# Optimization experiments

Measured on AMD Instinct MI355X. Metric: run time of the kernel, lower is better.

Reference implementation:

```python
import jax, jax.numpy as jnp
import numpy as np

N_NODES = 50000
N_EDGES = 640000
D = 128      # in_feats
OUT = 128    # out_feats


def setup_inputs() -> dict:
    key = jax.random.key(0)
    ks = jax.random.split(key, 8)
    feat = jax.random.normal(ks[0], (N_NODES, D), dtype=jnp.float32)
    weight = jax.random.uniform(ks[1], (N_EDGES,), dtype=jnp.float32)
    src = jax.random.randint(ks[2], (N_EDGES,), 0, N_NODES, dtype=jnp.int64)
    dst = jax.random.randint(ks[3], (N_EDGES,), 0, N_NODES, dtype=jnp.int64)
    # xavier_uniform with relu gain ~ sqrt(2)*sqrt(6/(fan_in+fan_out))
    g = np.sqrt(2.0)
    lim_pool = g * np.sqrt(6.0 / (D + D))
    lim_neigh = g * np.sqrt(6.0 / (2 * D + OUT))
    W_pool = jax.random.uniform(ks[4], (D, D), dtype=jnp.float32, minval=-lim_pool, maxval=lim_pool)
    b_pool = jnp.zeros((D,), dtype=jnp.float32)
    W_neigh = jax.random.uniform(ks[5], (OUT, 2 * D), dtype=jnp.float32, minval=-lim_neigh, maxval=lim_neigh)
    b_neigh = jnp.zeros((OUT,), dtype=jnp.float32)
    return {"feat": feat, "weight": weight, "src": src, "dst": dst,
            "W_pool": W_pool, "b_pool": b_pool, "W_neigh": W_neigh, "b_neigh": b_neigh}


def reference(feat, weight, src, dst, W_pool, b_pool, W_neigh, b_neigh):
    n = feat.shape[0]
    # fc_pool: h = feat @ W_pool.T + b_pool  -> [N, D]
    h = feat @ W_pool.T + b_pool
    # u_mul_e: per-edge message m_e = h[src_e] * w_e  -> [E, D]
    m = h[src] * weight[:, None]
    # max reduce over incoming edges (scatter-max by dst)
    neigh = jax.ops.segment_max(m, dst, num_segments=n)
    # zero-degree nodes get 0 (segment_max fills empties with -inf)
    deg = jax.ops.segment_sum(jnp.ones_like(weight), dst, num_segments=n)
    neigh = jnp.where(deg[:, None] > 0, neigh, jnp.zeros((), dtype=feat.dtype))
    # fc_neigh on concat(feat, neigh)
    rst = jnp.concatenate([feat, neigh], axis=1) @ W_neigh.T + b_neigh
    return rst
```

## Files before the change

### kernel.cpp

```cpp
#include <hip/hip_runtime.h>
#include <cstdint>
#include <cstddef>

#define N_NODES 50000
#define N_EDGES 640000
#define DF 128

#define NBUCK 196
#define BCAP  6144
#define PA_BLOCKS 250

typedef __attribute__((ext_vector_type(8))) short bf16x8;
typedef __attribute__((ext_vector_type(4))) float f32x4;

__device__ inline unsigned short f2bf(float f) {
    unsigned int u = __float_as_uint(f);
    return (unsigned short)((u + 0x7fffu + ((u >> 16) & 1u)) >> 16);
}

#define NF4 (N_NODES * DF / 4)
#define NWG (3 * 2048)
__global__ __launch_bounds__(256) void k1_setup_bucket(
    const float* __restrict__ feat,
    const float* __restrict__ W_pool,
    const float* __restrict__ W_neigh,
    const int* __restrict__ src,
    const int* __restrict__ dst,
    const float* __restrict__ w,
    unsigned short* __restrict__ featb,
    unsigned short* __restrict__ Wp_f,
    unsigned short* __restrict__ Wn1_f,
    unsigned short* __restrict__ Wn2_f,
    int* __restrict__ bucketcnt,
    uint2* __restrict__ staging)
{
    int bid = blockIdx.x;
    int t = threadIdx.x;
    if (bid < PA_BLOCKS) {
        __shared__ int cnt[NBUCK];
        __shared__ int runbase[NBUCK];
        int base = bid * 2560;
        if (t < NBUCK) cnt[t] = 0;
        __syncthreads();
        uint2 rec[10];
        int bk[10];
        #pragma unroll
        for (int i = 0; i < 10; ++i) {
            int e = base + i * 256 + t;
            int s = src[e], d = dst[e];
            bk[i] = d >> 8;
            rec[i].x = (unsigned int)s | ((unsigned int)(d & 255) << 16);
            rec[i].y = __float_as_uint(w[e]);
            atomicAdd(&cnt[bk[i]], 1);
        }
        __syncthreads();
        if (t < NBUCK) {
            runbase[t] = atomicAdd(&bucketcnt[t], cnt[t]);
            cnt[t] = 0;
        }
        __syncthreads();
        #pragma unroll
        for (int i = 0; i < 10; ++i) {
            int r = atomicAdd(&cnt[bk[i]], 1);
            int pos = runbase[bk[i]] + r;
            if (pos < BCAP) staging[bk[i] * BCAP + pos] = rec[i];
        }
    } else if (bid < 250 + NF4 / 256) {
        int idx = (bid - PA_BLOCKS) * 256 + t;
        float4 v = ((const float4*)feat)[idx];
        ushort4 o;
        o.x = f2bf(v.x); o.y = f2bf(v.y); o.z = f2bf(v.z); o.w = f2bf(v.w);
        ((ushort4*)featb)[idx] = o;
    } else {
        int g = (bid - PA_BLOCKS - NF4 / 256) * 256 + t;
        int m = g >> 11;
        int r8 = g & 2047;
        int L = r8 & 63, tt = (r8 >> 6) & 3, c = r8 >> 8;
        int o = c * 16 + (L & 15);
        int kb = tt * 32 + (L >> 4) * 8;
        const float* srcp;
        unsigned short* dstp;
        if (m == 0)      { srcp = W_pool  + o * 128 + kb;       dstp = Wp_f;  }
        else if (m == 1) { srcp = W_neigh + o * 256 + kb;       dstp = Wn1_f; }
        else             { srcp = W_neigh + o * 256 + 128 + kb; dstp = Wn2_f; }
        ushort4 lo, hi;
        float4 a = ((const float4*)srcp)[0];
        float4 b = ((const float4*)srcp)[1];
        lo.x = f2bf(a.x); lo.y = f2bf(a.y); lo.z = f2bf(a.z); lo.w = f2bf(a.w);
        hi.x = f2bf(b.x); hi.y = f2bf(b.y); hi.z = f2bf(b.z); hi.w = f2bf(b.w);
        ((ushort4*)(dstp + r8 * 8))[0] = lo;
        ((ushort4*)(dstp + r8 * 8))[1] = hi;
    }
}

#define GEMMB 196
__global__ __launch_bounds__(1024) void k2_gemm_passb(
    const unsigned short* __restrict__ featb,
    const unsigned short* __restrict__ Wp_f,
    const float* __restrict__ b_pool,
    unsigned short* __restrict__ hb,
    const int* __restrict__ bucketcnt,
    const uint2* __restrict__ staging,
    int* __restrict__ offsets,
    uint2* __restrict__ edges)
{
    int t = threadIdx.x;
    if (blockIdx.x < GEMMB) {
        int wave = blockIdx.x * 16 + (t >> 6);
        int lane = t & 63;
        int m0 = wave * 16;
        if (m0 >= N_NODES) return;
        const int n = lane & 15, quad = lane >> 4;

        f32x4 acc[8];
        #pragma unroll
        for (int c = 0; c < 8; ++c) {
            float bv = b_pool[c * 16 + n];
            acc[c] = (f32x4){bv, bv, bv, bv};
        }
        const unsigned short* aptr = featb + (size_t)(m0 + n) * DF + quad * 8;
        #pragma unroll
        for (int tt = 0; tt < 4; ++tt) {
            bf16x8 af = *(const bf16x8*)(aptr + tt * 32);
            #pragma unroll
            for (int c = 0; c < 8; ++c) {
                bf16x8 bf = *(const bf16x8*)(Wp_f + (size_t)((c * 4 + tt) * 64 + lane) * 8);
                acc[c] = __builtin_amdgcn_mfma_f32_16x16x32_bf16(af, bf, acc[c], 0, 0, 0);
            }
        }
        #pragma unroll
        for (int c = 0; c < 8; ++c)
            #pragma unroll
            for (int r = 0; r < 4; ++r)
                hb[(size_t)(m0 + quad * 4 + r) * DF + c * 16 + n] = f2bf(acc[c][r]);
    } else {
        __shared__ int dcnt[256];
        __shared__ int sc[256];
        __shared__ int bc[256];
        int b = blockIdx.x - GEMMB;

        if (t < 256) { dcnt[t] = 0; bc[t] = (t < NBUCK) ? bucketcnt[t] : 0; sc[t] = (t < NBUCK) ? bc[t] : 0; }
        __syncthreads();
        #pragma unroll
        for (int off = 1; off < 256; off <<= 1) {
            int u = (t < 256 && t >= off) ? sc[t - off] : 0;
            __syncthreads();
            if (t < 256) sc[t] += u;
            __syncthreads();
        }
        int mybase = (b > 0) ? sc[b - 1] : 0;
        int cnt = bc[b];
        __syncthreads();

        uint2 rec[6];
        int nit = (cnt + 1023) >> 10;
        for (int i = 0; i < nit; ++i) {
            int idx = i * 1024 + t;
            if (idx < cnt) {
                rec[i] = staging[(size_t)b * BCAP + idx];
                atomicAdd(&dcnt[(rec[i].x >> 16) & 255], 1);
            }
        }
        __syncthreads();
        if (t < 256) sc[t] = dcnt[t];
        __syncthreads();
        #pragma unroll
        for (int off = 1; off < 256; off <<= 1) {
            int u = (t < 256 && t >= off) ? sc[t - off] : 0;
            __syncthreads();
            if (t < 256) sc[t] += u;
            __syncthreads();
        }
        if (t < 256) {
            int node = b * 256 + t;
            int excl = sc[t] - dcnt[t];
            if (node < N_NODES) offsets[node] = mybase + excl;
            dcnt[t] = mybase + excl;
        }
        if (b == NBUCK - 1 && t == 0) offsets[N_NODES] = mybase + cnt;
        __syncthreads();
        for (int i = 0; i < nit; ++i) {
            int idx = i * 1024 + t;
            if (idx < cnt) {
                int dl = (rec[i].x >> 16) & 255;
                int pos = atomicAdd(&dcnt[dl], 1);
                uint2 fin;
                fin.x = rec[i].x & 0xFFFFu;
                fin.y = rec[i].y;
                edges[pos] = fin;
            }
        }
    }
}

__global__ __launch_bounds__(1024) void fused_max_out(
    const unsigned short* __restrict__ featb,
    const unsigned short* __restrict__ hb,
    const int* __restrict__ offsets,
    const uint2* __restrict__ edges,
    const unsigned short* __restrict__ Wn1_f,
    const unsigned short* __restrict__ Wn2_f,
    const float* __restrict__ bias,
    float* __restrict__ out)
{
    __shared__ __align__(16) unsigned short nsh[16 * DF];
    const int t = threadIdx.x;
    const int lane = t & 63;
    const int wid = t >> 6;
    const int m0 = blockIdx.x * 16;
    const int half = lane >> 5;
    const int q = lane & 31;

    const int node = __builtin_amdgcn_readfirstlane(m0 + wid);
    int beg = offsets[node], end = offsets[node + 1];
    float4 mx = make_float4(-3.4e38f, -3.4e38f, -3.4e38f, -3.4e38f);

    for (int e = beg; e < end; e += 8) {
        int i1 = min(e + 1, end - 1);
        int i2 = min(e + 2, end - 1);
        int i3 = min(e + 3, end - 1);
        int i4 = min(e + 4, end - 1);
        int i5 = min(e + 5, end - 1);
        int i6 = min(e + 6, end - 1);
        int i7 = min(e + 7, end - 1);
        uint2 e0 = edges[e],  e1 = edges[i1], e2 = edges[i2], e3 = edges[i3];
        uint2 e4 = edges[i4], e5 = edges[i5], e6 = edges[i6], e7 = edges[i7];
        uint2 mA = half ? e1 : e0;
        uint2 mB = half ? e3 : e2;
        uint2 mC = half ? e5 : e4;
        uint2 mD = half ? e7 : e6;
        float wA = __uint_as_float(mA.y);
        float wB = __uint_as_float(mB.y);
        float wC = __uint_as_float(mC.y);
        float wD = __uint_as_float(mD.y);
        uint2 pA = *(const uint2*)(hb + (size_t)mA.x * DF + q * 4);
        uint2 pB = *(const uint2*)(hb + (size_t)mB.x * DF + q * 4);
        uint2 pC = *(const uint2*)(hb + (size_t)mC.x * DF + q * 4);
        uint2 pD = *(const uint2*)(hb + (size_t)mD.x * DF + q * 4);
        mx.x = fmaxf(mx.x, __uint_as_float(pA.x << 16)          * wA);
        mx.y = fmaxf(mx.y, __uint_as_float(pA.x & 0xffff0000u)  * wA);
        mx.z = fmaxf(mx.z, __uint_as_float(pA.y << 16)          * wA);
        mx.w = fmaxf(mx.w, __uint_as_float(pA.y & 0xffff0000u)  * wA);
        mx.x = fmaxf(mx.x, __uint_as_float(pB.x << 16)          * wB);
        mx.y = fmaxf(mx.y, __uint_as_float(pB.x & 0xffff0000u)  * wB);
        mx.z = fmaxf(mx.z, __uint_as_float(pB.y << 16)          * wB);
        mx.w = fmaxf(mx.w, __uint_as_float(pB.y & 0xffff0000u)  * wB);
        mx.x = fmaxf(mx.x, __uint_as_float(pC.x << 16)          * wC);
        mx.y = fmaxf(mx.y, __uint_as_float(pC.x & 0xffff0000u)  * wC);
        mx.z = fmaxf(mx.z, __uint_as_float(pC.y << 16)          * wC);
        mx.w = fmaxf(mx.w, __uint_as_float(pC.y & 0xffff0000u)  * wC);
        mx.x = fmaxf(mx.x, __uint_as_float(pD.x << 16)          * wD);
        mx.y = fmaxf(mx.y, __uint_as_float(pD.x & 0xffff0000u)  * wD);
        mx.z = fmaxf(mx.z, __uint_as_float(pD.y << 16)          * wD);
        mx.w = fmaxf(mx.w, __uint_as_float(pD.y & 0xffff0000u)  * wD);
    }

    float4 o;
    o.x = fmaxf(mx.x, __shfl_xor(mx.x, 32));
    o.y = fmaxf(mx.y, __shfl_xor(mx.y, 32));
    o.z = fmaxf(mx.z, __shfl_xor(mx.z, 32));
    o.w = fmaxf(mx.w, __shfl_xor(mx.w, 32));
    if (beg == end) o = make_float4(0.f, 0.f, 0.f, 0.f);
    if (half == 0) {
        ushort4 ob;
        ob.x = f2bf(o.x); ob.y = f2bf(o.y); ob.z = f2bf(o.z); ob.w = f2bf(o.w);
        int boff = wid * 256 + ((q * 8) ^ ((wid & 7) << 4));
        *(ushort4*)((char*)nsh + boff) = ob;
    }

    const int n = lane & 15, quad = lane >> 4;
    f32x4 acc;
    if (wid < 8) {
        const int c = wid;
        float bv = bias[c * 16 + n];
        acc = (f32x4){bv, bv, bv, bv};
        const unsigned short* a0 = featb + (size_t)(m0 + n) * DF + quad * 8;
        #pragma unroll
        for (int tt = 0; tt < 4; ++tt) {
            bf16x8 af = *(const bf16x8*)(a0 + tt * 32);
            bf16x8 bfv = *(const bf16x8*)(Wn1_f + (size_t)((c * 4 + tt) * 64 + lane) * 8);
            acc = __builtin_amdgcn_mfma_f32_16x16x32_bf16(af, bfv, acc, 0, 0, 0);
        }
    }

    __syncthreads();
    if (wid >= 8) return;

    const int c = wid;
    #pragma unroll
    for (int tt = 0; tt < 4; ++tt) {
        int boff = (quad * 16 + tt * 64) ^ ((n & 7) << 4);
        bf16x8 af = *(const bf16x8*)((const char*)nsh + n * 256 + boff);
        bf16x8 bfv = *(const bf16x8*)(Wn2_f + (size_t)((c * 4 + tt) * 64 + lane) * 8);
        acc = __builtin_amdgcn_mfma_f32_16x16x32_bf16(af, bfv, acc, 0, 0, 0);
    }

    #pragma unroll
    for (int r = 0; r < 4; ++r)
        out[(size_t)(m0 + quad * 4 + r) * DF + c * 16 + n] = acc[r];
}

extern "C" void kernel_launch(void* const* d_in, const int* in_sizes, int n_in,
                              void* d_out, int out_size, void* d_ws, size_t ws_size,
                              hipStream_t stream) {
    const float* feat    = (const float*)d_in[0];
    const float* weight  = (const float*)d_in[1];
    const int*   src     = (const int*)d_in[2];
    const int*   dst     = (const int*)d_in[3];
    const float* W_pool  = (const float*)d_in[4];
    const float* b_pool  = (const float*)d_in[5];
    const float* W_neigh = (const float*)d_in[6];
    const float* b_neigh = (const float*)d_in[7];
    float* out = (float*)d_out;

    char* ws = (char*)d_ws;
    unsigned short* featb  = (unsigned short*)(ws);
    unsigned short* hb     = (unsigned short*)(ws + 12800000);
    unsigned short* Wp_f   = (unsigned short*)(ws + 38400000);
    unsigned short* Wn1_f  = (unsigned short*)(ws + 38432768);
    unsigned short* Wn2_f  = (unsigned short*)(ws + 38465536);
    int*   offsets   = (int*)  (ws + 38498304);
    int*   bucketcnt = (int*)  (ws + 38698368);
    uint2* staging   = (uint2*)(ws + 38699392);
    uint2* edges     = (uint2*)(ws + 48333184);

    hipMemsetAsync(bucketcnt, 0, 1024, stream);

    const int K1_BLOCKS = PA_BLOCKS + NF4 / 256 + NWG / 256;
    k1_setup_bucket<<<K1_BLOCKS, 256, 0, stream>>>(
        feat, W_pool, W_neigh, src, dst, weight,
        featb, Wp_f, Wn1_f, Wn2_f, bucketcnt, staging);

    k2_gemm_passb<<<GEMMB + NBUCK, 1024, 0, stream>>>(
        featb, Wp_f, b_pool, hb, bucketcnt, staging, offsets, edges);

    fused_max_out<<<N_NODES / 16, 1024, 0, stream>>>(
        featb, hb, offsets, edges, Wn1_f, Wn2_f, b_neigh, out);
}
```

Measured before the change: 163.4 us.

## Fuse feature bf16 conversion and pool GEMM into setup kernel

Moves the fc_pool GEMM out of the second kernel and into the first, where each block converts W_pool to bf16 in shared memory and converts feat rows on the fly, writing both featb and hb. This removes the separate featb round trip through global memory before the GEMM and leaves the second kernel doing only the bucket pass. In exchange, every GEMM block redundantly converts the whole 128x128 W_pool into 32KB of LDS, which adds per-block work and may limit occupancy.

After: 176.5 us. 1.08x slower.

```diff
diff --git a/kernel.cpp b/kernel.cpp
--- a/kernel.cpp
+++ b/kernel.cpp
@@ -9,6 +9,8 @@
 #define NBUCK 196
 #define BCAP  6144
 #define PA_BLOCKS 250
+#define GEMM_BLOCKS 782
+#define FRAG_BLOCKS 16
 
 typedef __attribute__((ext_vector_type(8))) short bf16x8;
 typedef __attribute__((ext_vector_type(4))) float f32x4;
@@ -18,17 +20,16 @@
     return (unsigned short)((u + 0x7fffu + ((u >> 16) & 1u)) >> 16);
 }
 
-#define NF4 (N_NODES * DF / 4)
-#define NWG (3 * 2048)
 __global__ __launch_bounds__(256) void k1_setup_bucket(
     const float* __restrict__ feat,
     const float* __restrict__ W_pool,
     const float* __restrict__ W_neigh,
+    const float* __restrict__ b_pool,
     const int* __restrict__ src,
     const int* __restrict__ dst,
     const float* __restrict__ w,
     unsigned short* __restrict__ featb,
-    unsigned short* __restrict__ Wp_f,
+    unsigned short* __restrict__ hb,
     unsigned short* __restrict__ Wn1_f,
     unsigned short* __restrict__ Wn2_f,
     int* __restrict__ bucketcnt,
@@ -65,24 +66,68 @@
             int pos = runbase[bk[i]] + r;
             if (pos < BCAP) staging[bk[i] * BCAP + pos] = rec[i];
         }
-    } else if (bid < 250 + NF4 / 256) {
-        int idx = (bid - PA_BLOCKS) * 256 + t;
-        float4 v = ((const float4*)feat)[idx];
-        ushort4 o;
-        o.x = f2bf(v.x); o.y = f2bf(v.y); o.z = f2bf(v.z); o.w = f2bf(v.w);
-        ((ushort4*)featb)[idx] = o;
+    } else if (bid < PA_BLOCKS + GEMM_BLOCKS) {
+        __shared__ __align__(16) unsigned short wsh[16384];
+        #pragma unroll
+        for (int k = 0; k < 8; ++k) {
+            int r8 = t * 8 + k;
+            int L = r8 & 63, tt2 = (r8 >> 6) & 3, c = r8 >> 8;
+            const float* srcp = W_pool + (c * 16 + (L & 15)) * 128
+                                       + tt2 * 32 + (L >> 4) * 8;
+            float4 a = ((const float4*)srcp)[0];
+            float4 b = ((const float4*)srcp)[1];
+            ushort4 lo, hi;
+            lo.x = f2bf(a.x); lo.y = f2bf(a.y); lo.z = f2bf(a.z); lo.w = f2bf(a.w);
+            hi.x = f2bf(b.x); hi.y = f2bf(b.y); hi.z = f2bf(b.z); hi.w = f2bf(b.w);
+            ((ushort4*)(wsh + r8 * 8))[0] = lo;
+            ((ushort4*)(wsh + r8 * 8))[1] = hi;
+        }
+        __syncthreads();
+
+        int gwave = (bid - PA_BLOCKS) * 4 + (t >> 6);
+        int m0 = gwave * 16;
+        if (m0 < N_NODES) {
+            int lane = t & 63;
+            const int n = lane & 15, quad = lane >> 4;
+            f32x4 acc[8];
+            #pragma unroll
+            for (int c = 0; c < 8; ++c) {
+                float bv = b_pool[c * 16 + n];
+                acc[c] = (f32x4){bv, bv, bv, bv};
+            }
+            const float* fp = feat + (size_t)(m0 + n) * DF + quad * 8;
+            unsigned short* fbp = featb + (size_t)(m0 + n) * DF + quad * 8;
+            #pragma unroll
+            for (int tt = 0; tt < 4; ++tt) {
+                float4 a = ((const float4*)(fp + tt * 32))[0];
+                float4 b = ((const float4*)(fp + tt * 32))[1];
+                union { bf16x8 v; ushort4 u4[2]; } af;
+                af.u4[0].x = f2bf(a.x); af.u4[0].y = f2bf(a.y);
+                af.u4[0].z = f2bf(a.z); af.u4[0].w = f2bf(a.w);
+                af.u4[1].x = f2bf(b.x); af.u4[1].y = f2bf(b.y);
+                af.u4[1].z = f2bf(b.z); af.u4[1].w = f2bf(b.w);
+                *(bf16x8*)(fbp + tt * 32) = af.v;
+                #pragma unroll
+                for (int c = 0; c < 8; ++c) {
+                    bf16x8 bfv = *(const bf16x8*)(wsh + (size_t)((c * 4 + tt) * 64 + lane) * 8);
+                    acc[c] = __builtin_amdgcn_mfma_f32_16x16x32_bf16(af.v, bfv, acc[c], 0, 0, 0);
+                }
+            }
+            #pragma unroll
+            for (int c = 0; c < 8; ++c)
+                #pragma unroll
+                for (int r = 0; r < 4; ++r)
+                    hb[(size_t)(m0 + quad * 4 + r) * DF + c * 16 + n] = f2bf(acc[c][r]);
+        }
     } else {
-        int g = (bid - PA_BLOCKS - NF4 / 256) * 256 + t;
+        int g = (bid - PA_BLOCKS - GEMM_BLOCKS) * 256 + t;
         int m = g >> 11;
         int r8 = g & 2047;
         int L = r8 & 63, tt = (r8 >> 6) & 3, c = r8 >> 8;
         int o = c * 16 + (L & 15);
         int kb = tt * 32 + (L >> 4) * 8;
-        const float* srcp;
-        unsigned short* dstp;
-        if (m == 0)      { srcp = W_pool  + o * 128 + kb;       dstp = Wp_f;  }
-        else if (m == 1) { srcp = W_neigh + o * 256 + kb;       dstp = Wn1_f; }
-        else             { srcp = W_neigh + o * 256 + 128 + kb; dstp = Wn2_f; }
+        const float* srcp = W_neigh + o * 256 + (m ? 128 : 0) + kb;
+        unsigned short* dstp = m ? Wn2_f : Wn1_f;
         ushort4 lo, hi;
         float4 a = ((const float4*)srcp)[0];
         float4 b = ((const float4*)srcp)[1];
@@ -93,102 +138,67 @@
     }
 }
 
-#define GEMMB 196
-__global__ __launch_bounds__(1024) void k2_gemm_passb(
-    const unsigned short* __restrict__ featb,
-    const unsigned short* __restrict__ Wp_f,
-    const float* __restrict__ b_pool,
-    unsigned short* __restrict__ hb,
+__global__ __launch_bounds__(1024) void k2_passb(
     const int* __restrict__ bucketcnt,
     const uint2* __restrict__ staging,
     int* __restrict__ offsets,
     uint2* __restrict__ edges)
 {
     int t = threadIdx.x;
-    if (blockIdx.x < GEMMB) {
-        int wave = blockIdx.x * 16 + (t >> 6);
-        int lane = t & 63;
-        int m0 = wave * 16;
-        if (m0 >= N_NODES) return;
-        const int n = lane & 15, quad = lane >> 4;
-
-        f32x4 acc[8];
-        #pragma unroll
-        for (int c = 0; c < 8; ++c) {
-            float bv = b_pool[c * 16 + n];
-            acc[c] = (f32x4){bv, bv, bv, bv};
-        }
-        const unsigned short* aptr = featb + (size_t)(m0 + n) * DF + quad * 8;
-        #pragma unroll
-        for (int tt = 0; tt < 4; ++tt) {
-            bf16x8 af = *(const bf16x8*)(aptr + tt * 32);
-            #pragma unroll
-            for (int c = 0; c < 8; ++c) {
-                bf16x8 bf = *(const bf16x8*)(Wp_f + (size_t)((c * 4 + tt) * 64 + lane) * 8);
-                acc[c] = __builtin_amdgcn_mfma_f32_16x16x32_bf16(af, bf, acc[c], 0, 0, 0);
-            }
-        }
-        #pragma unroll
-        for (int c = 0; c < 8; ++c)
-            #pragma unroll
-            for (int r = 0; r < 4; ++r)
-                hb[(size_t)(m0 + quad * 4 + r) * DF + c * 16 + n] = f2bf(acc[c][r]);
-    } else {
-        __shared__ int dcnt[256];
-        __shared__ int sc[256];
-        __shared__ int bc[256];
-        int b = blockIdx.x - GEMMB;
-
-        if (t < 256) { dcnt[t] = 0; bc[t] = (t < NBUCK) ? bucketcnt[t] : 0; sc[t] = (t < NBUCK) ? bc[t] : 0; }
-        __syncthreads();
-        #pragma unroll
-        for (int off = 1; off < 256; off <<= 1) {
-            int u = (t < 256 && t >= off) ? sc[t - off] : 0;
-            __syncthreads();
-            if (t < 256) sc[t] += u;
-            __syncthreads();
-        }
-        int mybase = (b > 0) ? sc[b - 1] : 0;
-        int cnt = bc[b];
-        __syncthreads();
-
-        uint2 rec[6];
-        int nit = (cnt + 1023) >> 10;
-        for (int i = 0; i < nit; ++i) {
-            int idx = i * 1024 + t;
-            if (idx < cnt) {
-                rec[i] = staging[(size_t)b * BCAP + idx];
-                atomicAdd(&dcnt[(rec[i].x >> 16) & 255], 1);
-            }
-        }
-        __syncthreads();
-        if (t < 256) sc[t] = dcnt[t];
-        __syncthreads();
-        #pragma unroll
-        for (int off = 1; off < 256; off <<= 1) {
-            int u = (t < 256 && t >= off) ? sc[t - off] : 0;
-            __syncthreads();
-            if (t < 256) sc[t] += u;
-            __syncthreads();
-        }
-        if (t < 256) {
-            int node = b * 256 + t;
-            int excl = sc[t] - dcnt[t];
-            if (node < N_NODES) offsets[node] = mybase + excl;
-            dcnt[t] = mybase + excl;
-        }
-        if (b == NBUCK - 1 && t == 0) offsets[N_NODES] = mybase + cnt;
-        __syncthreads();
-        for (int i = 0; i < nit; ++i) {
-            int idx = i * 1024 + t;
-            if (idx < cnt) {
-                int dl = (rec[i].x >> 16) & 255;
-                int pos = atomicAdd(&dcnt[dl], 1);
-                uint2 fin;
-                fin.x = rec[i].x & 0xFFFFu;
-                fin.y = rec[i].y;
-                edges[pos] = fin;
-            }
+    __shared__ int dcnt[256];
+    __shared__ int sc[256];
+    __shared__ int bc[256];
+    int b = blockIdx.x;
+
+    if (t < 256) { dcnt[t] = 0; bc[t] = (t < NBUCK) ? bucketcnt[t] : 0; sc[t] = (t < NBUCK) ? bc[t] : 0; }
+    __syncthreads();
+    #pragma unroll
+    for (int off = 1; off < 256; off <<= 1) {
+        int u = (t < 256 && t >= off) ? sc[t - off] : 0;
+        __syncthreads();
+        if (t < 256) sc[t] += u;
+        __syncthreads();
+    }
+    int mybase = (b > 0) ? sc[b - 1] : 0;
+    int cnt = bc[b];
+    __syncthreads();
+
+    uint2 rec[6];
+    int nit = (cnt + 1023) >> 10;
+    for (int i = 0; i < nit; ++i) {
+        int idx = i * 1024 + t;
+        if (idx < cnt) {
+            rec[i] = staging[(size_t)b * BCAP + idx];
+            atomicAdd(&dcnt[(rec[i].x >> 16) & 255], 1);
+        }
+    }
+    __syncthreads();
+    if (t < 256) sc[t] = dcnt[t];
+    __syncthreads();
+    #pragma unroll
+    for (int off = 1; off < 256; off <<= 1) {
+        int u = (t < 256 && t >= off) ? sc[t - off] : 0;
+        __syncthreads();
+        if (t < 256) sc[t] += u;
+        __syncthreads();
+    }
+    if (t < 256) {
+        int node = b * 256 + t;
+        int excl = sc[t] - dcnt[t];
+        if (node < N_NODES) offsets[node] = mybase + excl;
+        dcnt[t] = mybase + excl;
+    }
+    if (b == NBUCK - 1 && t == 0) offsets[N_NODES] = mybase + cnt;
+    __syncthreads();
+    for (int i = 0; i < nit; ++i) {
+        int idx = i * 1024 + t;
+        if (idx < cnt) {
+            int dl = (rec[i].x >> 16) & 255;
+            int pos = atomicAdd(&dcnt[dl], 1);
+            uint2 fin;
+            fin.x = rec[i].x & 0xFFFFu;
+            fin.y = rec[i].y;
+            edges[pos] = fin;
         }
     }
 }
@@ -316,7 +326,6 @@
     char* ws = (char*)d_ws;
     unsigned short* featb  = (unsigned short*)(ws);
     unsigned short* hb     = (unsigned short*)(ws + 12800000);
-    unsigned short* Wp_f   = (unsigned short*)(ws + 38400000);
     unsigned short* Wn1_f  = (unsigned short*)(ws + 38432768);
     unsigned short* Wn2_f  = (unsigned short*)(ws + 38465536);
     int*   offsets   = (int*)  (ws + 38498304);
@@ -326,13 +335,13 @@
 
     hipMemsetAsync(bucketcnt, 0, 1024, stream);
 
-    const int K1_BLOCKS = PA_BLOCKS + NF4 / 256 + NWG / 256;
+    const int K1_BLOCKS = PA_BLOCKS + GEMM_BLOCKS + FRAG_BLOCKS;
     k1_setup_bucket<<<K1_BLOCKS, 256, 0, stream>>>(
-        feat, W_pool, W_neigh, src, dst, weight,
-        featb, Wp_f, Wn1_f, Wn2_f, bucketcnt, staging);
-
-    k2_gemm_passb<<<GEMMB + NBUCK, 1024, 0, stream>>>(
-        featb, Wp_f, b_pool, hb, bucketcnt, staging, offsets, edges);
+        feat, W_pool, W_neigh, b_pool, src, dst, weight,
+        featb, hb, Wn1_f, Wn2_f, bucketcnt, staging);
+
+    k2_passb<<<NBUCK, 1024, 0, stream>>>(
+        bucketcnt, staging, offsets, edges);
 
     fused_max_out<<<N_NODES / 16, 1024, 0, stream>>>(
         featb, hb, offsets, edges, Wn1_f, Wn2_f, b_neigh, out);
```

## Pad per-node edge lists to multiples of eight with dummy edges

Applied to the files above, without the earlier changes.

Each node's CSR edge list is padded to a multiple of 8 using dummy edges that point at a sentinel row of hb filled with a very negative bf16 value, so the max-aggregation loop can drop its per-edge clamped index computation. Buckets now use fixed ECAP-sized regions with a separate end array, which removes the global prefix scan over bucket counts in the pass-B blocks. In exchange, extra padded edges are read, and the design depends on each bucket's padded total fitting within ECAP.

Result: no change. 163.3 us (-0.0%).

```diff
diff --git a/kernel.cpp b/kernel.cpp
--- a/kernel.cpp
+++ b/kernel.cpp
@@ -8,7 +8,9 @@
 
 #define NBUCK 196
 #define BCAP  6144
+#define ECAP  8192
 #define PA_BLOCKS 250
+#define DUMMY_ROW 50000
 
 typedef __attribute__((ext_vector_type(8))) short bf16x8;
 typedef __attribute__((ext_vector_type(4))) float f32x4;
@@ -28,6 +30,7 @@
     const int* __restrict__ dst,
     const float* __restrict__ w,
     unsigned short* __restrict__ featb,
+    unsigned short* __restrict__ hb,
     unsigned short* __restrict__ Wp_f,
     unsigned short* __restrict__ Wn1_f,
     unsigned short* __restrict__ Wn2_f,
@@ -71,7 +74,7 @@
         ushort4 o;
         o.x = f2bf(v.x); o.y = f2bf(v.y); o.z = f2bf(v.z); o.w = f2bf(v.w);
         ((ushort4*)featb)[idx] = o;
-    } else {
+    } else if (bid < 250 + NF4 / 256 + NWG / 256) {
         int g = (bid - PA_BLOCKS - NF4 / 256) * 256 + t;
         int m = g >> 11;
         int r8 = g & 2047;
@@ -90,6 +93,8 @@
         hi.x = f2bf(b.x); hi.y = f2bf(b.y); hi.z = f2bf(b.z); hi.w = f2bf(b.w);
         ((ushort4*)(dstp + r8 * 8))[0] = lo;
         ((ushort4*)(dstp + r8 * 8))[1] = hi;
+    } else {
+        if (t < DF) hb[(size_t)DUMMY_ROW * DF + t] = 0xFF7Fu;
     }
 }
 
@@ -102,6 +107,7 @@
     const int* __restrict__ bucketcnt,
     const uint2* __restrict__ staging,
     int* __restrict__ offsets,
+    int* __restrict__ nend,
     uint2* __restrict__ edges)
 {
     int t = threadIdx.x;
@@ -136,20 +142,11 @@
     } else {
         __shared__ int dcnt[256];
         __shared__ int sc[256];
-        __shared__ int bc[256];
         int b = blockIdx.x - GEMMB;
-
-        if (t < 256) { dcnt[t] = 0; bc[t] = (t < NBUCK) ? bucketcnt[t] : 0; sc[t] = (t < NBUCK) ? bc[t] : 0; }
-        __syncthreads();
-        #pragma unroll
-        for (int off = 1; off < 256; off <<= 1) {
-            int u = (t < 256 && t >= off) ? sc[t - off] : 0;
-            __syncthreads();
-            if (t < 256) sc[t] += u;
-            __syncthreads();
-        }
-        int mybase = (b > 0) ? sc[b - 1] : 0;
-        int cnt = bc[b];
+        int cnt = bucketcnt[b];
+        if (cnt > BCAP) cnt = BCAP;
+
+        if (t < 256) dcnt[t] = 0;
         __syncthreads();
 
         uint2 rec[6];
@@ -162,7 +159,12 @@
             }
         }
         __syncthreads();
-        if (t < 256) sc[t] = dcnt[t];
+        int mydeg = 0, mypad = 0;
+        if (t < 256) {
+            mydeg = dcnt[t];
+            mypad = (mydeg + 7) & ~7;
+            sc[t] = mypad;
+        }
         __syncthreads();
         #pragma unroll
         for (int off = 1; off < 256; off <<= 1) {
@@ -172,12 +174,16 @@
             __syncthreads();
         }
         if (t < 256) {
+            int beg = b * ECAP + sc[t] - mypad;
             int node = b * 256 + t;
-            int excl = sc[t] - dcnt[t];
-            if (node < N_NODES) offsets[node] = mybase + excl;
-            dcnt[t] = mybase + excl;
-        }
-        if (b == NBUCK - 1 && t == 0) offsets[N_NODES] = mybase + cnt;
+            if (node < N_NODES) {
+                offsets[node] = beg;
+                nend[node] = beg + mypad;
+            }
+            dcnt[t] = beg;
+            uint2 dmy; dmy.x = DUMMY_ROW; dmy.y = 0x3F800000u;
+            for (int k = mydeg; k < mypad; ++k) edges[beg + k] = dmy;
+        }
         __syncthreads();
         for (int i = 0; i < nit; ++i) {
             int idx = i * 1024 + t;
@@ -197,6 +203,7 @@
     const unsigned short* __restrict__ featb,
     const unsigned short* __restrict__ hb,
     const int* __restrict__ offsets,
+    const int* __restrict__ nend,
     const uint2* __restrict__ edges,
     const unsigned short* __restrict__ Wn1_f,
     const unsigned short* __restrict__ Wn2_f,
@@ -212,19 +219,12 @@
     const int q = lane & 31;
 
     const int node = __builtin_amdgcn_readfirstlane(m0 + wid);
-    int beg = offsets[node], end = offsets[node + 1];
+    int beg = offsets[node], end = nend[node];
     float4 mx = make_float4(-3.4e38f, -3.4e38f, -3.4e38f, -3.4e38f);
 
     for (int e = beg; e < end; e += 8) {
-        int i1 = min(e + 1, end - 1);
-        int i2 = min(e + 2, end - 1);
-        int i3 = min(e + 3, end - 1);
-        int i4 = min(e + 4, end - 1);
-        int i5 = min(e + 5, end - 1);
-        int i6 = min(e + 6, end - 1);
-        int i7 = min(e + 7, end - 1);
-        uint2 e0 = edges[e],  e1 = edges[i1], e2 = edges[i2], e3 = edges[i3];
-        uint2 e4 = edges[i4], e5 = edges[i5], e6 = edges[i6], e7 = edges[i7];
+        uint2 e0 = edges[e],     e1 = edges[e + 1], e2 = edges[e + 2], e3 = edges[e + 3];
+        uint2 e4 = edges[e + 4], e5 = edges[e + 5], e6 = edges[e + 6], e7 = edges[e + 7];
         uint2 mA = half ? e1 : e0;
         uint2 mB = half ? e3 : e2;
         uint2 mC = half ? e5 : e4;
@@ -316,24 +316,25 @@
     char* ws = (char*)d_ws;
     unsigned short* featb  = (unsigned short*)(ws);
     unsigned short* hb     = (unsigned short*)(ws + 12800000);
-    unsigned short* Wp_f   = (unsigned short*)(ws + 38400000);
-    unsigned short* Wn1_f  = (unsigned short*)(ws + 38432768);
-    unsigned short* Wn2_f  = (unsigned short*)(ws + 38465536);
-    int*   offsets   = (int*)  (ws + 38498304);
-    int*   bucketcnt = (int*)  (ws + 38698368);
-    uint2* staging   = (uint2*)(ws + 38699392);
-    uint2* edges     = (uint2*)(ws + 48333184);
+    unsigned short* Wp_f   = (unsigned short*)(ws + 25600512);
+    unsigned short* Wn1_f  = (unsigned short*)(ws + 25633280);
+    unsigned short* Wn2_f  = (unsigned short*)(ws + 25666048);
+    int*   offsets   = (int*)  (ws + 25698816);
+    int*   nend      = (int*)  (ws + 25898816);
+    int*   bucketcnt = (int*)  (ws + 26098816);
+    uint2* staging   = (uint2*)(ws + 26099840);
+    uint2* edges     = (uint2*)(ws + 35733632);
 
     hipMemsetAsync(bucketcnt, 0, 1024, stream);
 
-    const int K1_BLOCKS = PA_BLOCKS + NF4 / 256 + NWG / 256;
+    const int K1_BLOCKS = PA_BLOCKS + NF4 / 256 + NWG / 256 + 1;
     k1_setup_bucket<<<K1_BLOCKS, 256, 0, stream>>>(
         feat, W_pool, W_neigh, src, dst, weight,
-        featb, Wp_f, Wn1_f, Wn2_f, bucketcnt, staging);
+        featb, hb, Wp_f, Wn1_f, Wn2_f, bucketcnt, staging);
 
     k2_gemm_passb<<<GEMMB + NBUCK, 1024, 0, stream>>>(
-        featb, Wp_f, b_pool, hb, bucketcnt, staging, offsets, edges);
+        featb, Wp_f, b_pool, hb, bucketcnt, staging, offsets, nend, edges);
 
     fused_max_out<<<N_NODES / 16, 1024, 0, stream>>>(
-        featb, hb, offsets, edges, Wn1_f, Wn2_f, b_neigh, out);
-}
+        featb, hb, offsets, nend, edges, Wn1_f, Wn2_f, b_neigh, out);
+}
```
